# Optimization experiments

Hardware: AMD Instinct MI355X
Metric: run time of the kernel (lower is better)

Reference implementation:

```python
import jax, jax.numpy as jnp
import numpy as np
from jax import lax

B, N, K = 8, 4096, 16          # clouds, points per cloud, knn neighbors
RATIO = 0.5
M = int(N * RATIO)             # sampled points per cloud (fps ratio)
C_IN, C_OUT = 64, 128
EPS = 1e-5                      # BatchNorm eps


def setup_inputs() -> dict:
    key = jax.random.key(0)
    ks = jax.random.split(key, 4)
    x = jax.random.normal(ks[0], (B * N, C_IN), jnp.float32)
    pos = jax.random.uniform(ks[1], (B * N, 3), jnp.float32)
    batch = jnp.repeat(jnp.arange(B, dtype=jnp.int32), N)
    W = jax.random.normal(ks[2], (C_IN, C_OUT), jnp.float32) / np.sqrt(C_IN).astype(np.float32)
    b = jnp.zeros((C_OUT,), jnp.float32)
    gamma = jnp.ones((C_OUT,), jnp.float32)
    beta = jnp.zeros((C_OUT,), jnp.float32)
    return {"x": x, "pos": pos, "batch": batch, "W": W, "b": b, "gamma": gamma, "beta": beta}


def _fps(pos_c):
    # Farthest point sampling on one cloud. pos_c: [N,3] -> [M] local indices.
    # Deterministic start at index 0 (reference for torch_cluster.fps).
    def step(carry, _):
        dmin, last = carry
        d = jnp.sum((pos_c - pos_c[last]) ** 2, axis=-1)   # [N]
        dmin = jnp.minimum(dmin, d)
        nxt = jnp.argmax(dmin).astype(jnp.int32)
        return (dmin, nxt), last
    init = (jnp.full((pos_c.shape[0],), jnp.inf, pos_c.dtype), jnp.int32(0))
    _, idx = lax.scan(step, init, None, length=M)
    return idx


def _knn(pos_c, qpos_c):
    # k nearest original points for each sampled point. [N,3],[M,3] -> [M,K].
    d = jnp.sum((qpos_c[:, None, :] - pos_c[None, :, :]) ** 2, axis=-1)  # [M,N]
    _, idx = lax.top_k(-d, K)
    return idx


def reference(x, pos, batch, W, b, gamma, beta):
    pos_b = pos.reshape(B, N, 3)
    fps_idx = jax.vmap(_fps)(pos_b)                                       # [B,M]
    new_pos_b = jnp.take_along_axis(pos_b, fps_idx[:, :, None], axis=1)   # [B,M,3]
    nbr = jax.vmap(_knn)(pos_b, new_pos_b)                                # [B,M,K]

    # mlp: Linear -> BatchNorm1d (training-mode batch stats) -> GELU
    h = x @ W + b                                                         # [B*N,C_OUT]
    mu = jnp.mean(h, axis=0)
    var = jnp.mean((h - mu) ** 2, axis=0)
    h = (h - mu) * lax.rsqrt(var + EPS) * gamma + beta
    h = jax.nn.gelu(h, approximate=False)
    h_b = h.reshape(B, N, C_OUT)

    # gather neighbor features; scatter-max over edge_index[0] == max over K
    # (each sampled point has exactly K incoming edges)
    feats = jax.vmap(lambda hb, nb: hb[nb])(h_b, nbr)                     # [B,M,K,C_OUT]
    new_x = jnp.max(feats, axis=2).reshape(B * M, C_OUT)
    new_pos = new_pos_b.reshape(B * M, 3)
    new_batch = jnp.repeat(jnp.arange(B, dtype=batch.dtype), M)
    return (new_x, new_pos, new_batch)
```

## Files before the change

kernel.cpp:

```cpp
#include <hip/hip_runtime.h>
#include <math.h>

#define NB 8
#define NN 4096
#define MM 2048
#define KNN_K 16
#define CIN 64
#define COUT 128
#define BN_EPS 1e-5f

typedef float v2f __attribute__((ext_vector_type(2)));

__device__ __forceinline__ v2f pk_add(v2f a, v2f b) {
  v2f r;
  asm("v_pk_add_f32 %0, %1, %2" : "=v"(r) : "v"(a), "v"(b));
  return r;
}
__device__ __forceinline__ v2f pk_mul(v2f a, v2f b) {
  v2f r;
  asm("v_pk_mul_f32 %0, %1, %2" : "=v"(r) : "v"(a), "v"(b));
  return r;
}

__device__ __forceinline__ double pack_key(float d, unsigned code) {
  return __longlong_as_double(
      (long long)(((unsigned long long)__float_as_uint(d) << 32) | code));
}
__device__ __forceinline__ unsigned unpack_code(double v) {
  return (unsigned)((unsigned long long)__double_as_longlong(v) &
                    0xFFFFFFFFull);
}

__device__ __forceinline__ float sqdist_np(float dx, float dy, float dz) {
  return __fadd_rn(__fadd_rn(__fmul_rn(dx, dx), __fmul_rn(dy, dy)),
                   __fmul_rn(dz, dz));
}

#define DPP_MAX_LEVEL(best, ctrl, rmask)                                     \
  {                                                                          \
    const int _lo = __builtin_amdgcn_update_dpp(                             \
        __double2loint(best), __double2loint(best), (ctrl), (rmask), 0xf,    \
        false);                                                              \
    const int _hi = __builtin_amdgcn_update_dpp(                             \
        __double2hiint(best), __double2hiint(best), (ctrl), (rmask), 0xf,    \
        false);                                                              \
    best = fmax(best, __hiloint2double(_hi, _lo));                           \
  }

__global__ __launch_bounds__(256) void k_fps_gemm(
    const float* __restrict__ pos, const float* __restrict__ x,
    const float* __restrict__ W, const float* __restrict__ bias,
    float* __restrict__ h, float* __restrict__ gsum,
    float* __restrict__ gsumsq, int* __restrict__ fps_idx,
    float* __restrict__ out_pos, float* __restrict__ out_batch) {
  __shared__ __align__(16) char smem_raw[57472];
  const int tid = threadIdx.x;

  if (blockIdx.x < NB) {
    float* xs = (float*)smem_raw;
    float* ys = xs + NN;
    float* zs = ys + NN;
    int* idxs = (int*)(smem_raw + 49152);
    double* red = (double*)(smem_raw + 57344);
    const int b = blockIdx.x;
    const float* posc = pos + (size_t)b * NN * 3;
    for (int i = tid; i < NN; i += 256) {
      xs[i] = posc[i * 3 + 0];
      ys[i] = posc[i * 3 + 1];
      zs[i] = posc[i * 3 + 2];
    }
    __syncthreads();

    v2f pxv[8], pyv[8], pzv[8];
    double key[16];
    const unsigned code_base = (unsigned)(NN - 1 - tid * 16);
#pragma unroll
    for (int u = 0; u < 8; ++u) {
      const int p = tid * 16 + 2 * u;
      pxv[u] = (v2f){xs[p], xs[p + 1]};
      pyv[u] = (v2f){ys[p], ys[p + 1]};
      pzv[u] = (v2f){zs[p], zs[p + 1]};
    }
#pragma unroll
    for (int s = 0; s < 16; ++s)
      key[s] = __hiloint2double(0x7f800000, (int)(code_base - s));

    const int lane = tid & 63, wv = tid >> 6;
    int last = 0;
    if (tid == 0) idxs[0] = 0;
    float lx = xs[0], ly = ys[0], lz = zs[0];
    for (int m = 1; m < MM; ++m) {
      const v2f nlx = {-lx, -lx}, nly = {-ly, -ly}, nlz = {-lz, -lz};
      double b0 = 0.0, b1 = 0.0, b2 = 0.0, b3 = 0.0;
#pragma unroll
      for (int u = 0; u < 8; ++u) {
        const v2f dx = pk_add(pxv[u], nlx);
        const v2f dy = pk_add(pyv[u], nly);
        const v2f dz = pk_add(pzv[u], nlz);
        const v2f d2 =
            pk_add(pk_add(pk_mul(dx, dx), pk_mul(dy, dy)), pk_mul(dz, dz));
        const int s0 = 2 * u, s1 = 2 * u + 1;
        const float n0 =
            fminf(__int_as_float(__double2hiint(key[s0])), d2.x);
        const float n1 =
            fminf(__int_as_float(__double2hiint(key[s1])), d2.y);
        key[s0] = __hiloint2double(__float_as_int(n0), (int)(code_base - s0));
        key[s1] = __hiloint2double(__float_as_int(n1), (int)(code_base - s1));
        switch (u & 3) {
          case 0: b0 = fmax(b0, fmax(key[s0], key[s1])); break;
          case 1: b1 = fmax(b1, fmax(key[s0], key[s1])); break;
          case 2: b2 = fmax(b2, fmax(key[s0], key[s1])); break;
          default: b3 = fmax(b3, fmax(key[s0], key[s1])); break;
        }
      }
      double best = fmax(fmax(b0, b1), fmax(b2, b3));
      DPP_MAX_LEVEL(best, 0x121, 0xf);
      DPP_MAX_LEVEL(best, 0x122, 0xf);
      DPP_MAX_LEVEL(best, 0x124, 0xf);
      DPP_MAX_LEVEL(best, 0x128, 0xf);
      DPP_MAX_LEVEL(best, 0x142, 0xa);
      DPP_MAX_LEVEL(best, 0x143, 0xc);
      const int par = (m & 1) * 4;
      if (lane == 63) red[par + wv] = best;
      __syncthreads();
      const double f = fmax(fmax(red[par + 0], red[par + 1]),
                            fmax(red[par + 2], red[par + 3]));
      last = (NN - 1) - (int)unpack_code(f);
      if (tid == 0) idxs[m] = last;
      lx = xs[last];
      ly = ys[last];
      lz = zs[last];
    }
    __syncthreads();
    for (int m = tid; m < MM; m += 256) {
      const int p = idxs[m];
      const int o = b * MM + m;
      fps_idx[o] = p;
      out_pos[o * 3 + 0] = xs[p];
      out_pos[o * 3 + 1] = ys[p];
      out_pos[o * 3 + 2] = zs[p];
      out_batch[o] = (float)b;
    }
  } else {
    float* Wl = (float*)smem_raw;
    float* xl = Wl + CIN * COUT;
    float* bsum = (float*)(smem_raw + 49152);
    float* bsq = bsum + COUT;
    const int bid = blockIdx.x - NB;
    const int r0 = bid * 64;
    for (int i = tid; i < CIN * COUT; i += 256) Wl[i] = W[i];
    for (int i = tid; i < 64 * CIN; i += 256) xl[i] = x[(size_t)r0 * CIN + i];
    if (tid < COUT) {
      bsum[tid] = 0.f;
      bsq[tid] = 0.f;
    }
    __syncthreads();
    const int cg = tid & 31, rg = tid >> 5;
    const int c = cg * 4;
    float acc[8][4];
#pragma unroll
    for (int j = 0; j < 8; ++j)
#pragma unroll
      for (int t = 0; t < 4; ++t) acc[j][t] = 0.f;
    for (int k = 0; k < CIN; ++k) {
      const float4 wk = *(const float4*)&Wl[k * COUT + c];
#pragma unroll
      for (int j = 0; j < 8; ++j) {
        const float xv = xl[(rg * 8 + j) * CIN + k];
        acc[j][0] = fmaf(xv, wk.x, acc[j][0]);
        acc[j][1] = fmaf(xv, wk.y, acc[j][1]);
        acc[j][2] = fmaf(xv, wk.z, acc[j][2]);
        acc[j][3] = fmaf(xv, wk.w, acc[j][3]);
      }
    }
    const float4 bb = *(const float4*)&bias[c];
    float s0 = 0, s1 = 0, s2 = 0, s3 = 0, q0 = 0, q1 = 0, q2 = 0, q3 = 0;
#pragma unroll
    for (int j = 0; j < 8; ++j) {
      float4 hv;
      hv.x = acc[j][0] + bb.x;
      hv.y = acc[j][1] + bb.y;
      hv.z = acc[j][2] + bb.z;
      hv.w = acc[j][3] + bb.w;
      *(float4*)&h[(size_t)(r0 + rg * 8 + j) * COUT + c] = hv;
      s0 += hv.x; s1 += hv.y; s2 += hv.z; s3 += hv.w;
      q0 += hv.x * hv.x; q1 += hv.y * hv.y;
      q2 += hv.z * hv.z; q3 += hv.w * hv.w;
    }
    atomicAdd(&bsum[c + 0], s0); atomicAdd(&bsum[c + 1], s1);
    atomicAdd(&bsum[c + 2], s2); atomicAdd(&bsum[c + 3], s3);
    atomicAdd(&bsq[c + 0], q0);  atomicAdd(&bsq[c + 1], q1);
    atomicAdd(&bsq[c + 2], q2);  atomicAdd(&bsq[c + 3], q3);
    __syncthreads();
    if (tid < COUT) {
      atomicAdd(&gsum[tid], bsum[tid]);
      atomicAdd(&gsumsq[tid], bsq[tid]);
    }
  }
}

__device__ __forceinline__ float gelu_exact(float v) {
  return 0.5f * v * (1.0f + erff(v * 0.70710678118654752f));
}

__global__ __launch_bounds__(256) void k_act(float* __restrict__ h,
                                             const float* __restrict__ gsum,
                                             const float* __restrict__ gsumsq,
                                             const float* __restrict__ gamma,
                                             const float* __restrict__ beta) {
  __shared__ float sc[COUT], sh[COUT];
  const int t = threadIdx.x;
  if (t < COUT) {
    const float n = (float)(NB * NN);
    const float mu = gsum[t] / n;
    const float var = gsumsq[t] / n - mu * mu;
    const float rs = rsqrtf(var + BN_EPS);
    const float s = rs * gamma[t];
    sc[t] = s;
    sh[t] = beta[t] - mu * s;
  }
  __syncthreads();
  const int g = blockIdx.x * 256 + t;
  const int c = (g & 31) * 4;
  float4* h4 = (float4*)h;
  float4 v = h4[g];
  const float4 s4 = *(const float4*)&sc[c];
  const float4 b4 = *(const float4*)&sh[c];
  v.x = gelu_exact(v.x * s4.x + b4.x);
  v.y = gelu_exact(v.y * s4.y + b4.y);
  v.z = gelu_exact(v.z * s4.z + b4.z);
  v.w = gelu_exact(v.w * s4.w + b4.w);
  h4[g] = v;
}

__global__ __launch_bounds__(256) void k_knn(const float* __restrict__ pos,
                                             const int* __restrict__ fps_idx,
                                             const float* __restrict__ h,
                                             float* __restrict__ out_x) {
  __shared__ float dc[4][NN];
  const int tid = threadIdx.x, lane = tid & 63, wv = tid >> 6;
  const int q = blockIdx.x * 4 + wv;
  const int b = q >> 11, m = q & (MM - 1);
  const int qi = fps_idx[b * MM + m];
  const float* posc = pos + (size_t)b * NN * 3;
  const float qx = posc[qi * 3 + 0], qy = posc[qi * 3 + 1],
              qz = posc[qi * 3 + 2];
  float* dcw = dc[wv];
  const double DINF = __longlong_as_double(0x7FF0000000000000LL);
  double gmin[8];
#pragma unroll
  for (int g = 0; g < 8; ++g) gmin[g] = DINF;
#pragma unroll
  for (int s = 0; s < 64; ++s) {
    const int p = s * 64 + lane;
    const float d = sqdist_np(posc[p * 3 + 0] - qx, posc[p * 3 + 1] - qy,
                              posc[p * 3 + 2] - qz);
    dcw[p] = d;
    gmin[s >> 3] = fmin(gmin[s >> 3], pack_key(d, (unsigned)p));
  }
  double lmin = gmin[0];
#pragma unroll
  for (int g = 1; g < 8; ++g) lmin = fmin(lmin, gmin[g]);

  int nbr[KNN_K];
#pragma unroll
  for (int r = 0; r < KNN_K; ++r) {
    double v = lmin;
#pragma unroll
    for (int off = 32; off; off >>= 1) v = fmin(v, __shfl_xor(v, off, 64));
    const unsigned p = unpack_code(v);
    nbr[r] = (int)p;
    if (lane == (int)(p & 63)) {
      dcw[p] = __int_as_float(0x7f800000);
      const int g = (int)(p >> 9);
      double nm = DINF;
      const int base = g * 8 * 64 + lane;
#pragma unroll
      for (int j = 0; j < 8; ++j) {
        const int pp = base + j * 64;
        nm = fmin(nm, pack_key(dcw[pp], (unsigned)pp));
      }
#pragma unroll
      for (int gg = 0; gg < 8; ++gg)
        if (gg == g) gmin[gg] = nm;
      lmin = gmin[0];
#pragma unroll
      for (int gg = 1; gg < 8; ++gg) lmin = fmin(lmin, gmin[gg]);
    }
  }

  const float* hb = h + (size_t)b * NN * COUT;
  float f0 = -__int_as_float(0x7f800000), f1 = f0;
#pragma unroll
  for (int r = 0; r < KNN_K; ++r) {
    const float* row = hb + (size_t)nbr[r] * COUT;
    f0 = fmaxf(f0, row[lane]);
    f1 = fmaxf(f1, row[lane + 64]);
  }
  out_x[(size_t)q * COUT + lane] = f0;
  out_x[(size_t)q * COUT + lane + 64] = f1;
}

extern "C" void kernel_launch(void* const* d_in, const int* in_sizes, int n_in,
                              void* d_out, int out_size, void* d_ws,
                              size_t ws_size, hipStream_t stream) {
  const float* x = (const float*)d_in[0];
  const float* pos = (const float*)d_in[1];
  const float* W = (const float*)d_in[3];
  const float* bias = (const float*)d_in[4];
  const float* gamma = (const float*)d_in[5];
  const float* beta = (const float*)d_in[6];

  float* out_x = (float*)d_out;
  float* out_pos = out_x + (size_t)NB * MM * COUT;
  float* out_batch = out_pos + (size_t)NB * MM * 3;

  char* ws = (char*)d_ws;
  float* h = (float*)ws;
  float* gsum = (float*)(ws + (size_t)16777216);
  float* gsumsq = gsum + COUT;
  int* fps_idx = (int*)(gsumsq + COUT);

  (void)hipMemsetAsync(gsum, 0, 2 * COUT * sizeof(float), stream);
  hipLaunchKernelGGL(k_fps_gemm, dim3(NB + 512), dim3(256), 0, stream, pos, x,
                     W, bias, h, gsum, gsumsq, fps_idx, out_pos, out_batch);
  hipLaunchKernelGGL(k_act, dim3(4096), dim3(256), 0, stream, h, gsum, gsumsq,
                     gamma, beta);
  hipLaunchKernelGGL(k_knn, dim3(4096), dim3(256), 0, stream, pos, fps_idx, h,
                     out_x);
}
```

Measured before the change: 1.240 ms.

## Widen FPS blocks to 512 threads with float dmin and late index selection

The FPS block goes from 256 to 512 threads, so each thread owns 8 points instead of 16. Per-point state changes from packed double keys to plain float minimum distances, and the packed (distance, index) key is built once per step after a float max and a select. Positions move to a float4-padded shared layout so the chosen point is read with a single vector load. The GEMM half is retiled to 4 rows per thread to match the larger block. The cost is an 8-wave cross-wave reduction per step, more shared memory per block, and lower occupancy for the GEMM blocks.

```diff
diff --git a/kernel.cpp b/kernel.cpp
--- a/kernel.cpp
+++ b/kernel.cpp
@@ -8,6 +8,8 @@
 #define CIN 64
 #define COUT 128
 #define BN_EPS 1e-5f
+#define FPS_THR 512
+#define PTS 8
 
 typedef float v2f __attribute__((ext_vector_type(2)));
 
@@ -47,98 +49,95 @@
     best = fmax(best, __hiloint2double(_hi, _lo));                           \
   }
 
-__global__ __launch_bounds__(256) void k_fps_gemm(
+__global__ __launch_bounds__(512) void k_fps_gemm(
     const float* __restrict__ pos, const float* __restrict__ x,
     const float* __restrict__ W, const float* __restrict__ bias,
     float* __restrict__ h, float* __restrict__ gsum,
     float* __restrict__ gsumsq, int* __restrict__ fps_idx,
     float* __restrict__ out_pos, float* __restrict__ out_batch) {
-  __shared__ __align__(16) char smem_raw[57472];
+  __shared__ __align__(16) char smem_raw[73856];
   const int tid = threadIdx.x;
 
   if (blockIdx.x < NB) {
-    float* xs = (float*)smem_raw;
-    float* ys = xs + NN;
-    float* zs = ys + NN;
-    int* idxs = (int*)(smem_raw + 49152);
-    double* red = (double*)(smem_raw + 57344);
+    float* pos4 = (float*)smem_raw;
+    int* idxs = (int*)(smem_raw + 65536);
+    double* red = (double*)(smem_raw + 73728);
     const int b = blockIdx.x;
     const float* posc = pos + (size_t)b * NN * 3;
-    for (int i = tid; i < NN; i += 256) {
-      xs[i] = posc[i * 3 + 0];
-      ys[i] = posc[i * 3 + 1];
-      zs[i] = posc[i * 3 + 2];
+    for (int p = tid; p < NN; p += FPS_THR) {
+      pos4[4 * p + 0] = posc[3 * p + 0];
+      pos4[4 * p + 1] = posc[3 * p + 1];
+      pos4[4 * p + 2] = posc[3 * p + 2];
+    }
+    if (tid == 0) idxs[0] = 0;
+
+    v2f pxv[4], pyv[4], pzv[4];
+    float dmin[PTS];
+    const int p0 = tid * PTS;
+    const unsigned code_base = (unsigned)(NN - 1 - p0);
+#pragma unroll
+    for (int u = 0; u < 4; ++u) {
+      const int p = p0 + 2 * u;
+      pxv[u] = (v2f){posc[3 * p + 0], posc[3 * p + 3]};
+      pyv[u] = (v2f){posc[3 * p + 1], posc[3 * p + 4]};
+      pzv[u] = (v2f){posc[3 * p + 2], posc[3 * p + 5]};
+      dmin[2 * u] = __int_as_float(0x7f800000);
+      dmin[2 * u + 1] = __int_as_float(0x7f800000);
     }
     __syncthreads();
-
-    v2f pxv[8], pyv[8], pzv[8];
-    double key[16];
-    const unsigned code_base = (unsigned)(NN - 1 - tid * 16);
-#pragma unroll
-    for (int u = 0; u < 8; ++u) {
-      const int p = tid * 16 + 2 * u;
-      pxv[u] = (v2f){xs[p], xs[p + 1]};
-      pyv[u] = (v2f){ys[p], ys[p + 1]};
-      pzv[u] = (v2f){zs[p], zs[p + 1]};
-    }
-#pragma unroll
-    for (int s = 0; s < 16; ++s)
-      key[s] = __hiloint2double(0x7f800000, (int)(code_base - s));
-
     const int lane = tid & 63, wv = tid >> 6;
-    int last = 0;
-    if (tid == 0) idxs[0] = 0;
-    float lx = xs[0], ly = ys[0], lz = zs[0];
+    float lx = pos4[0], ly = pos4[1], lz = pos4[2];
     for (int m = 1; m < MM; ++m) {
       const v2f nlx = {-lx, -lx}, nly = {-ly, -ly}, nlz = {-lz, -lz};
-      double b0 = 0.0, b1 = 0.0, b2 = 0.0, b3 = 0.0;
-#pragma unroll
-      for (int u = 0; u < 8; ++u) {
+#pragma unroll
+      for (int u = 0; u < 4; ++u) {
         const v2f dx = pk_add(pxv[u], nlx);
         const v2f dy = pk_add(pyv[u], nly);
         const v2f dz = pk_add(pzv[u], nlz);
         const v2f d2 =
             pk_add(pk_add(pk_mul(dx, dx), pk_mul(dy, dy)), pk_mul(dz, dz));
-        const int s0 = 2 * u, s1 = 2 * u + 1;
-        const float n0 =
-            fminf(__int_as_float(__double2hiint(key[s0])), d2.x);
-        const float n1 =
-            fminf(__int_as_float(__double2hiint(key[s1])), d2.y);
-        key[s0] = __hiloint2double(__float_as_int(n0), (int)(code_base - s0));
-        key[s1] = __hiloint2double(__float_as_int(n1), (int)(code_base - s1));
-        switch (u & 3) {
-          case 0: b0 = fmax(b0, fmax(key[s0], key[s1])); break;
-          case 1: b1 = fmax(b1, fmax(key[s0], key[s1])); break;
-          case 2: b2 = fmax(b2, fmax(key[s0], key[s1])); break;
-          default: b3 = fmax(b3, fmax(key[s0], key[s1])); break;
-        }
+        dmin[2 * u] = fminf(dmin[2 * u], d2.x);
+        dmin[2 * u + 1] = fminf(dmin[2 * u + 1], d2.y);
       }
-      double best = fmax(fmax(b0, b1), fmax(b2, b3));
+      const float M =
+          fmaxf(fmaxf(fmaxf(fmaxf(dmin[0], dmin[1]), fmaxf(dmin[2], dmin[3])),
+                      fmaxf(dmin[4], dmin[5])),
+                fmaxf(dmin[6], dmin[7]));
+      unsigned sel = code_base - 7;
+#pragma unroll
+      for (int s = 6; s >= 0; --s)
+        sel = (dmin[s] == M) ? (code_base - s) : sel;
+      double best = pack_key(M, sel);
       DPP_MAX_LEVEL(best, 0x121, 0xf);
       DPP_MAX_LEVEL(best, 0x122, 0xf);
       DPP_MAX_LEVEL(best, 0x124, 0xf);
       DPP_MAX_LEVEL(best, 0x128, 0xf);
       DPP_MAX_LEVEL(best, 0x142, 0xa);
       DPP_MAX_LEVEL(best, 0x143, 0xc);
-      const int par = (m & 1) * 4;
+      const int par = (m & 1) * 8;
       if (lane == 63) red[par + wv] = best;
       __syncthreads();
-      const double f = fmax(fmax(red[par + 0], red[par + 1]),
-                            fmax(red[par + 2], red[par + 3]));
-      last = (NN - 1) - (int)unpack_code(f);
+      const double2* rp = (const double2*)&red[par];
+      const double2 r0 = rp[0], r1 = rp[1], r2 = rp[2], r3 = rp[3];
+      const double f =
+          fmax(fmax(fmax(r0.x, r0.y), fmax(r1.x, r1.y)),
+               fmax(fmax(r2.x, r2.y), fmax(r3.x, r3.y)));
+      const int last = (NN - 1) - (int)unpack_code(f);
       if (tid == 0) idxs[m] = last;
-      lx = xs[last];
-      ly = ys[last];
-      lz = zs[last];
+      const float4 lp = *(const float4*)&pos4[4 * last];
+      lx = lp.x;
+      ly = lp.y;
+      lz = lp.z;
     }
     __syncthreads();
-    for (int m = tid; m < MM; m += 256) {
+    for (int m = tid; m < MM; m += FPS_THR) {
       const int p = idxs[m];
       const int o = b * MM + m;
+      const float4 pp = *(const float4*)&pos4[4 * p];
       fps_idx[o] = p;
-      out_pos[o * 3 + 0] = xs[p];
-      out_pos[o * 3 + 1] = ys[p];
-      out_pos[o * 3 + 2] = zs[p];
+      out_pos[o * 3 + 0] = pp.x;
+      out_pos[o * 3 + 1] = pp.y;
+      out_pos[o * 3 + 2] = pp.z;
       out_batch[o] = (float)b;
     }
   } else {
@@ -148,25 +147,23 @@
     float* bsq = bsum + COUT;
     const int bid = blockIdx.x - NB;
     const int r0 = bid * 64;
-    for (int i = tid; i < CIN * COUT; i += 256) Wl[i] = W[i];
-    for (int i = tid; i < 64 * CIN; i += 256) xl[i] = x[(size_t)r0 * CIN + i];
-    if (tid < COUT) {
-      bsum[tid] = 0.f;
-      bsq[tid] = 0.f;
-    }
+    for (int i = tid; i < CIN * COUT; i += FPS_THR) Wl[i] = W[i];
+    for (int i = tid; i < 64 * CIN; i += FPS_THR)
+      xl[i] = x[(size_t)r0 * CIN + i];
+    if (tid < 2 * COUT) ((float*)(smem_raw + 49152))[tid] = 0.f;
     __syncthreads();
     const int cg = tid & 31, rg = tid >> 5;
     const int c = cg * 4;
-    float acc[8][4];
-#pragma unroll
-    for (int j = 0; j < 8; ++j)
+    float acc[4][4];
+#pragma unroll
+    for (int j = 0; j < 4; ++j)
 #pragma unroll
       for (int t = 0; t < 4; ++t) acc[j][t] = 0.f;
     for (int k = 0; k < CIN; ++k) {
       const float4 wk = *(const float4*)&Wl[k * COUT + c];
 #pragma unroll
-      for (int j = 0; j < 8; ++j) {
-        const float xv = xl[(rg * 8 + j) * CIN + k];
+      for (int j = 0; j < 4; ++j) {
+        const float xv = xl[(rg * 4 + j) * CIN + k];
         acc[j][0] = fmaf(xv, wk.x, acc[j][0]);
         acc[j][1] = fmaf(xv, wk.y, acc[j][1]);
         acc[j][2] = fmaf(xv, wk.z, acc[j][2]);
@@ -176,13 +173,13 @@
     const float4 bb = *(const float4*)&bias[c];
     float s0 = 0, s1 = 0, s2 = 0, s3 = 0, q0 = 0, q1 = 0, q2 = 0, q3 = 0;
 #pragma unroll
-    for (int j = 0; j < 8; ++j) {
+    for (int j = 0; j < 4; ++j) {
       float4 hv;
       hv.x = acc[j][0] + bb.x;
       hv.y = acc[j][1] + bb.y;
       hv.z = acc[j][2] + bb.z;
       hv.w = acc[j][3] + bb.w;
-      *(float4*)&h[(size_t)(r0 + rg * 8 + j) * COUT + c] = hv;
+      *(float4*)&h[(size_t)(r0 + rg * 4 + j) * COUT + c] = hv;
       s0 += hv.x; s1 += hv.y; s2 += hv.z; s3 += hv.w;
       q0 += hv.x * hv.x; q1 += hv.y * hv.y;
       q2 += hv.z * hv.z; q3 += hv.w * hv.w;
@@ -322,8 +319,8 @@
   int* fps_idx = (int*)(gsumsq + COUT);
 
   (void)hipMemsetAsync(gsum, 0, 2 * COUT * sizeof(float), stream);
-  hipLaunchKernelGGL(k_fps_gemm, dim3(NB + 512), dim3(256), 0, stream, pos, x,
-                     W, bias, h, gsum, gsumsq, fps_idx, out_pos, out_batch);
+  hipLaunchKernelGGL(k_fps_gemm, dim3(NB + 512), dim3(FPS_THR), 0, stream, pos,
+                     x, W, bias, h, gsum, gsumsq, fps_idx, out_pos, out_batch);
   hipLaunchKernelGGL(k_act, dim3(4096), dim3(256), 0, stream, h, gsum, gsumsq,
                      gamma, beta);
   hipLaunchKernelGGL(k_knn, dim3(4096), dim3(256), 0, stream, pos, fps_idx, h,
```

After: 1.428 ms. 1.15x slower.

## Replace FPS block barrier with sentinel-slot spin sync and DPP kNN reduction

Applied to the files above, without the earlier changes.

In the farthest-point-sampling loop, the per-iteration __syncthreads is replaced by a triple-buffered LDS slot scheme. Each wave publishes its max key, spins until all four slots are no longer the sentinel, then resets a slot from an older buffer. The kNN top-k min reduction now uses DPP row/broadcast ops plus readlane instead of shfl_xor butterflies. The spin relies on volatile LDS ordering between waves, which risks subtle races, and busy-waiting can contend with the other waves.

```diff
diff --git a/kernel.cpp b/kernel.cpp
--- a/kernel.cpp
+++ b/kernel.cpp
@@ -8,6 +8,7 @@
 #define CIN 64
 #define COUT 128
 #define BN_EPS 1e-5f
+#define SENT 0xFFFFFFFFFFFFFFFFull
 
 typedef float v2f __attribute__((ext_vector_type(2)));
 
@@ -46,6 +47,16 @@
         false);                                                              \
     best = fmax(best, __hiloint2double(_hi, _lo));                           \
   }
+#define DPP_MIN_LEVEL(best, ctrl, rmask)                                     \
+  {                                                                          \
+    const int _lo = __builtin_amdgcn_update_dpp(                             \
+        __double2loint(best), __double2loint(best), (ctrl), (rmask), 0xf,    \
+        false);                                                              \
+    const int _hi = __builtin_amdgcn_update_dpp(                             \
+        __double2hiint(best), __double2hiint(best), (ctrl), (rmask), 0xf,    \
+        false);                                                              \
+    best = fmin(best, __hiloint2double(_hi, _lo));                           \
+  }
 
 __global__ __launch_bounds__(256) void k_fps_gemm(
     const float* __restrict__ pos, const float* __restrict__ x,
@@ -61,7 +72,9 @@
     float* ys = xs + NN;
     float* zs = ys + NN;
     int* idxs = (int*)(smem_raw + 49152);
-    double* red = (double*)(smem_raw + 57344);
+    unsigned long long* slot =
+        (unsigned long long*)(smem_raw + 57344);
+    volatile unsigned long long* vslot = (volatile unsigned long long*)slot;
     const int b = blockIdx.x;
     const float* posc = pos + (size_t)b * NN * 3;
     for (int i = tid; i < NN; i += 256) {
@@ -69,6 +82,7 @@
       ys[i] = posc[i * 3 + 1];
       zs[i] = posc[i * 3 + 2];
     }
+    if (tid < 12) slot[tid] = SENT;
     __syncthreads();
 
     v2f pxv[8], pyv[8], pzv[8];
@@ -86,9 +100,9 @@
       key[s] = __hiloint2double(0x7f800000, (int)(code_base - s));
 
     const int lane = tid & 63, wv = tid >> 6;
-    int last = 0;
     if (tid == 0) idxs[0] = 0;
     float lx = xs[0], ly = ys[0], lz = zs[0];
+    int par = 1;
     for (int m = 1; m < MM; ++m) {
       const v2f nlx = {-lx, -lx}, nly = {-ly, -ly}, nlz = {-lz, -lz};
       double b0 = 0.0, b1 = 0.0, b2 = 0.0, b3 = 0.0;
@@ -120,12 +134,25 @@
       DPP_MAX_LEVEL(best, 0x128, 0xf);
       DPP_MAX_LEVEL(best, 0x142, 0xa);
       DPP_MAX_LEVEL(best, 0x143, 0xc);
-      const int par = (m & 1) * 4;
-      if (lane == 63) red[par + wv] = best;
-      __syncthreads();
-      const double f = fmax(fmax(red[par + 0], red[par + 1]),
-                            fmax(red[par + 2], red[par + 3]));
-      last = (NN - 1) - (int)unpack_code(f);
+      const int pb = par * 4;
+      if (lane == 63)
+        vslot[pb + wv] = (unsigned long long)__double_as_longlong(best);
+      unsigned long long k0, k1, k2, k3;
+      do {
+        k0 = vslot[pb + 0];
+        k1 = vslot[pb + 1];
+        k2 = vslot[pb + 2];
+        k3 = vslot[pb + 3];
+      } while (k0 == SENT || k1 == SENT || k2 == SENT || k3 == SENT);
+      par = (par == 2) ? 0 : par + 1;
+      if (lane == 63) vslot[(((pb >> 2) + 2) % 3) * 4 + wv] = SENT;
+      __threadfence_block();
+      const double f =
+          fmax(fmax(__longlong_as_double((long long)k0),
+                    __longlong_as_double((long long)k1)),
+               fmax(__longlong_as_double((long long)k2),
+                    __longlong_as_double((long long)k3)));
+      const int last = (NN - 1) - (int)unpack_code(f);
       if (tid == 0) idxs[m] = last;
       lx = xs[last];
       ly = ys[last];
@@ -150,10 +177,7 @@
     const int r0 = bid * 64;
     for (int i = tid; i < CIN * COUT; i += 256) Wl[i] = W[i];
     for (int i = tid; i < 64 * CIN; i += 256) xl[i] = x[(size_t)r0 * CIN + i];
-    if (tid < COUT) {
-      bsum[tid] = 0.f;
-      bsq[tid] = 0.f;
-    }
+    if (tid < 2 * COUT) bsum[tid] = 0.f;
     __syncthreads();
     const int cg = tid & 31, rg = tid >> 5;
     const int c = cg * 4;
@@ -266,9 +290,14 @@
 #pragma unroll
   for (int r = 0; r < KNN_K; ++r) {
     double v = lmin;
-#pragma unroll
-    for (int off = 32; off; off >>= 1) v = fmin(v, __shfl_xor(v, off, 64));
-    const unsigned p = unpack_code(v);
+    DPP_MIN_LEVEL(v, 0x121, 0xf);
+    DPP_MIN_LEVEL(v, 0x122, 0xf);
+    DPP_MIN_LEVEL(v, 0x124, 0xf);
+    DPP_MIN_LEVEL(v, 0x128, 0xf);
+    DPP_MIN_LEVEL(v, 0x142, 0xa);
+    DPP_MIN_LEVEL(v, 0x143, 0xc);
+    const unsigned p =
+        (unsigned)__builtin_amdgcn_readlane(__double2loint(v), 63);
     nbr[r] = (int)p;
     if (lane == (int)(p & 63)) {
       dcw[p] = __int_as_float(0x7f800000);
```

After: 1.619 ms. +30.6%, slower.

## Fuse BatchNorm+GELU into KNN max-gather using max/min extrema; DPP min reduction

Applied to the files above, without the earlier changes.

Drops the separate activation kernel that read and rewrote the full hidden matrix. The KNN kernel now tracks both the max and min of the raw pre-norm features over the 16 neighbours and applies the affine BatchNorm and GELU only to those two values, taking the larger result. This works because the affine map is monotone, and GELU has a single minimum, so the maximum over a set is reached at one of its extremes. It also replaces the shuffle-xor wavefront min reduction with DPP row operations plus a readlane, and reorders block-to-query mapping to interleave clouds.

```diff
diff --git a/kernel.cpp b/kernel.cpp
--- a/kernel.cpp
+++ b/kernel.cpp
@@ -45,6 +45,16 @@
         __double2hiint(best), __double2hiint(best), (ctrl), (rmask), 0xf,    \
         false);                                                              \
     best = fmax(best, __hiloint2double(_hi, _lo));                           \
+  }
+#define DPP_MIN_LEVEL(best, ctrl, rmask)                                     \
+  {                                                                          \
+    const int _lo = __builtin_amdgcn_update_dpp(                             \
+        __double2loint(best), __double2loint(best), (ctrl), (rmask), 0xf,    \
+        false);                                                              \
+    const int _hi = __builtin_amdgcn_update_dpp(                             \
+        __double2hiint(best), __double2hiint(best), (ctrl), (rmask), 0xf,    \
+        false);                                                              \
+    best = fmin(best, __hiloint2double(_hi, _lo));                           \
   }
 
 __global__ __launch_bounds__(256) void k_fps_gemm(
@@ -150,10 +160,7 @@
     const int r0 = bid * 64;
     for (int i = tid; i < CIN * COUT; i += 256) Wl[i] = W[i];
     for (int i = tid; i < 64 * CIN; i += 256) xl[i] = x[(size_t)r0 * CIN + i];
-    if (tid < COUT) {
-      bsum[tid] = 0.f;
-      bsq[tid] = 0.f;
-    }
+    if (tid < 2 * COUT) bsum[tid] = 0.f;
     __syncthreads();
     const int cg = tid & 31, rg = tid >> 5;
     const int c = cg * 4;
@@ -203,45 +210,28 @@
   return 0.5f * v * (1.0f + erff(v * 0.70710678118654752f));
 }
 
-__global__ __launch_bounds__(256) void k_act(float* __restrict__ h,
-                                             const float* __restrict__ gsum,
-                                             const float* __restrict__ gsumsq,
-                                             const float* __restrict__ gamma,
-                                             const float* __restrict__ beta) {
+__global__ __launch_bounds__(256) void k_knn(
+    const float* __restrict__ pos, const int* __restrict__ fps_idx,
+    const float* __restrict__ h, const float* __restrict__ gsum,
+    const float* __restrict__ gsumsq, const float* __restrict__ gamma,
+    const float* __restrict__ beta, float* __restrict__ out_x) {
+  __shared__ float dc[4][NN];
   __shared__ float sc[COUT], sh[COUT];
-  const int t = threadIdx.x;
-  if (t < COUT) {
+  const int tid = threadIdx.x, lane = tid & 63, wv = tid >> 6;
+  if (tid < COUT) {
     const float n = (float)(NB * NN);
-    const float mu = gsum[t] / n;
-    const float var = gsumsq[t] / n - mu * mu;
+    const float mu = gsum[tid] / n;
+    const float var = gsumsq[tid] / n - mu * mu;
     const float rs = rsqrtf(var + BN_EPS);
-    const float s = rs * gamma[t];
-    sc[t] = s;
-    sh[t] = beta[t] - mu * s;
+    const float s = rs * gamma[tid];
+    sc[tid] = s;
+    sh[tid] = beta[tid] - mu * s;
   }
   __syncthreads();
-  const int g = blockIdx.x * 256 + t;
-  const int c = (g & 31) * 4;
-  float4* h4 = (float4*)h;
-  float4 v = h4[g];
-  const float4 s4 = *(const float4*)&sc[c];
-  const float4 b4 = *(const float4*)&sh[c];
-  v.x = gelu_exact(v.x * s4.x + b4.x);
-  v.y = gelu_exact(v.y * s4.y + b4.y);
-  v.z = gelu_exact(v.z * s4.z + b4.z);
-  v.w = gelu_exact(v.w * s4.w + b4.w);
-  h4[g] = v;
-}
-
-__global__ __launch_bounds__(256) void k_knn(const float* __restrict__ pos,
-                                             const int* __restrict__ fps_idx,
-                                             const float* __restrict__ h,
-                                             float* __restrict__ out_x) {
-  __shared__ float dc[4][NN];
-  const int tid = threadIdx.x, lane = tid & 63, wv = tid >> 6;
-  const int q = blockIdx.x * 4 + wv;
-  const int b = q >> 11, m = q & (MM - 1);
-  const int qi = fps_idx[b * MM + m];
+  const int b = blockIdx.x & 7;
+  const int m = (blockIdx.x >> 3) * 4 + wv;
+  const int q = b * MM + m;
+  const int qi = fps_idx[q];
   const float* posc = pos + (size_t)b * NN * 3;
   const float qx = posc[qi * 3 + 0], qy = posc[qi * 3 + 1],
               qz = posc[qi * 3 + 2];
@@ -266,9 +256,14 @@
 #pragma unroll
   for (int r = 0; r < KNN_K; ++r) {
     double v = lmin;
-#pragma unroll
-    for (int off = 32; off; off >>= 1) v = fmin(v, __shfl_xor(v, off, 64));
-    const unsigned p = unpack_code(v);
+    DPP_MIN_LEVEL(v, 0x121, 0xf);
+    DPP_MIN_LEVEL(v, 0x122, 0xf);
+    DPP_MIN_LEVEL(v, 0x124, 0xf);
+    DPP_MIN_LEVEL(v, 0x128, 0xf);
+    DPP_MIN_LEVEL(v, 0x142, 0xa);
+    DPP_MIN_LEVEL(v, 0x143, 0xc);
+    const unsigned p =
+        (unsigned)__builtin_amdgcn_readlane(__double2loint(v), 63);
     nbr[r] = (int)p;
     if (lane == (int)(p & 63)) {
       dcw[p] = __int_as_float(0x7f800000);
@@ -290,15 +285,25 @@
   }
 
   const float* hb = h + (size_t)b * NN * COUT;
-  float f0 = -__int_as_float(0x7f800000), f1 = f0;
+  const float PINF = __int_as_float(0x7f800000);
+  float mx0 = -PINF, mn0 = PINF, mx1 = -PINF, mn1 = PINF;
 #pragma unroll
   for (int r = 0; r < KNN_K; ++r) {
     const float* row = hb + (size_t)nbr[r] * COUT;
-    f0 = fmaxf(f0, row[lane]);
-    f1 = fmaxf(f1, row[lane + 64]);
-  }
-  out_x[(size_t)q * COUT + lane] = f0;
-  out_x[(size_t)q * COUT + lane + 64] = f1;
+    const float a = row[lane], c = row[lane + 64];
+    mx0 = fmaxf(mx0, a);
+    mn0 = fminf(mn0, a);
+    mx1 = fmaxf(mx1, c);
+    mn1 = fminf(mn1, c);
+  }
+  const float sc0 = sc[lane], sh0 = sh[lane];
+  const float sc1 = sc[lane + 64], sh1 = sh[lane + 64];
+  const float o0 = fmaxf(gelu_exact(fmaf(mx0, sc0, sh0)),
+                         gelu_exact(fmaf(mn0, sc0, sh0)));
+  const float o1 = fmaxf(gelu_exact(fmaf(mx1, sc1, sh1)),
+                         gelu_exact(fmaf(mn1, sc1, sh1)));
+  out_x[(size_t)q * COUT + lane] = o0;
+  out_x[(size_t)q * COUT + lane + 64] = o1;
 }
 
 extern "C" void kernel_launch(void* const* d_in, const int* in_sizes, int n_in,
@@ -324,8 +329,6 @@
   (void)hipMemsetAsync(gsum, 0, 2 * COUT * sizeof(float), stream);
   hipLaunchKernelGGL(k_fps_gemm, dim3(NB + 512), dim3(256), 0, stream, pos, x,
                      W, bias, h, gsum, gsumsq, fps_idx, out_pos, out_batch);
-  hipLaunchKernelGGL(k_act, dim3(4096), dim3(256), 0, stream, h, gsum, gsumsq,
-                     gamma, beta);
   hipLaunchKernelGGL(k_knn, dim3(4096), dim3(256), 0, stream, pos, fps_idx, h,
-                     out_x);
-}
+                     gsum, gsumsq, gamma, beta, out_x);
+}
```

Result: no change. 1.237 ms (-0.2%).
